# Optimization experiments

Measured on AMD Instinct MI355X. Metric: run time of the kernel, lower is better.

Reference implementation:

```python
import jax, jax.numpy as jnp
import numpy as np

L = 3            # max degree for L_in = L_edge = L_out = (0, 3)
B = 1024         # batch (number of edges)
C_IN = 256
C_OUT = 256
NUM_ORDERS = (L + 1) ** 2  # 16


def _build_structure(L):
    """Rebuild the coo_CG sparse structure: nonzeros sorted by (M_out, l1, l2),
    using the CG selection rule m1 + m2 = m for valid triangle triples."""
    triples = {}
    for l1 in range(L + 1):
        for l2 in range(L + 1):
            for l in range(abs(l1 - l2), min(L, l1 + l2) + 1):
                key = (l, l1, l2)
                if key not in triples:
                    triples[key] = len(triples)
    M1, M2, seg1, lind_g, seg2 = [], [], [], [], []
    g = 0
    for l in range(L + 1):
        for m in range(-l, l + 1):
            M = l * l + l + m  # flat order index of (l, m)
            for (lo, l1, l2) in sorted(triples.keys()):
                if lo != l:
                    continue
                cnt = 0
                for m1 in range(-l1, l1 + 1):
                    m2 = m - m1
                    if -l2 <= m2 <= l2:
                        M1.append(l1 * l1 + l1 + m1)
                        M2.append(l2 * l2 + l2 + m2)
                        seg1.append(g)
                        cnt += 1
                if cnt > 0:
                    lind_g.append(triples[(lo, l1, l2)])
                    seg2.append(M)
                    g += 1
    return (np.asarray(M1, np.int32), np.asarray(M2, np.int32),
            np.asarray(seg1, np.int32), np.asarray(lind_g, np.int32),
            np.asarray(seg2, np.int32), len(triples), g)


def setup_inputs() -> dict:
    key = jax.random.key(0)
    k1, k2, k3, k4 = jax.random.split(key, 4)
    M1, M2, seg1, l_ind, seg2, n_w, n_g = _build_structure(L)
    # expected: 478 nnz, 156 groups, 34 weights
    x = jax.random.normal(k1, (B, NUM_ORDERS, C_IN), jnp.float32)
    sh = jax.random.normal(k2, (B, NUM_ORDERS), jnp.float32)
    fan = np.sqrt(2.0 / (C_IN + C_OUT)).astype(np.float32)
    weight = jax.random.normal(k3, (n_w, C_IN, C_OUT), jnp.float32) * fan
    CG_vals = jax.random.normal(k4, (M1.shape[0],), jnp.float32) * 0.3
    return {
        'x': x, 'sh': sh, 'weight': weight, 'CG_vals': CG_vals,
        'M1': jnp.asarray(M1), 'M2': jnp.asarray(M2), 'seg1': jnp.asarray(seg1),
        'l_ind': jnp.asarray(l_ind), 'seg2': jnp.asarray(seg2),
        'num_orders_out': NUM_ORDERS,
    }


def reference(x, sh, weight, CG_vals, M1, M2, seg1, l_ind, seg2, num_orders_out):
    # x: (B, Mi, Ci); sh: (B, Me); weight: (num_weights, Ci, Co)
    Bn = x.shape[0]
    G = l_ind.shape[0]
    Ci = x.shape[-1]
    Co = weight.shape[-1]
    feat = x[:, M1, :]                                      # (B, nnz, Ci) gather on orders
    sh_g = sh[:, M2]                                        # (B, nnz)
    inter = (CG_vals[None, :] * sh_g)[..., None] * feat     # (B, nnz, Ci)
    inter = jnp.zeros((Bn, G, Ci), x.dtype).at[:, seg1, :].add(inter)   # segment over (M,l1,l2)
    w = weight[l_ind]                                       # (G, Ci, Co)
    ret = jnp.einsum('bgi,gio->bgo', inter, w)              # per-group matmul
    out = jnp.zeros((Bn, num_orders_out, Co), x.dtype).at[:, seg2, :].add(ret)  # segment over M
    return out
```

## Files before the change

### kernel.cpp

```cpp
#include <hip/hip_runtime.h>
#include <stdint.h>

#define B_SZ 1024
#define NO   16
#define CI   256
#define CO   256
#define BK   64
#define BM   32
#define LDB  72
#define LDAA 264
#define MAXG 12
#define MAXE 48
#define WP   76

typedef unsigned short u16;
typedef __attribute__((ext_vector_type(8))) short short8;
typedef __attribute__((ext_vector_type(4))) float f32x4;
typedef __attribute__((ext_vector_type(4))) unsigned short u16x4;
typedef __attribute__((ext_vector_type(8))) unsigned short u16x8;

__device__ __forceinline__ u16 f2bf(float f) {
  union { float f; uint32_t u; } v; v.f = f;
  uint32_t u = v.u;
  return (u16)((u + 0x7FFFu + ((u >> 16) & 1u)) >> 16);
}
__device__ __forceinline__ float bf2f(u16 h) {
  union { float f; uint32_t u; } v; v.u = ((uint32_t)h) << 16; return v.f;
}

__device__ __forceinline__ f32x4 mfma_16x16x32_bf16(short8 a, short8 b, f32x4 c) {
  asm volatile("v_mfma_f32_16x16x32_bf16 %0, %1, %2, %0" : "+v"(c) : "v"(a), "v"(b));
  return c;
}

extern "C" __global__ void xconv_kernel(const float* __restrict__ x,
                                        u16* __restrict__ xbf, int n8) {
  int t = blockIdx.x * 256 + threadIdx.x;
  if (t >= n8) return;
  const float* s = x + (size_t)t * 8;
  float4 a = ((const float4*)s)[0];
  float4 b = ((const float4*)s)[1];
  u16x8 pk;
  pk[0] = f2bf(a.x); pk[1] = f2bf(a.y); pk[2] = f2bf(a.z); pk[3] = f2bf(a.w);
  pk[4] = f2bf(b.x); pk[5] = f2bf(b.y); pk[6] = f2bf(b.z); pk[7] = f2bf(b.w);
  *(u16x8*)(xbf + (size_t)t * 8) = pk;
}

extern "C" __global__ void wconv_kernel(const float* __restrict__ w,
                                        u16* __restrict__ wbf) {
  __shared__ u16 t_lds[64 * WP];
  const int tid = threadIdx.x;
  const int bid = blockIdx.x;
  const int wi = bid >> 4;
  const int i0 = ((bid >> 2) & 3) * 64;
  const int o0 = (bid & 3) * 64;
  const float* src = w + (size_t)wi * (CI * CO);
  u16* dst = wbf + (size_t)wi * (CI * CO);
#pragma unroll
  for (int p = 0; p < 4; ++p) {
    int idx = p * 256 + tid;
    int i = idx >> 4, oq = (idx & 15) * 4;
    float4 v = *(const float4*)(src + (size_t)(i0 + i) * CO + o0 + oq);
    t_lds[(oq + 0) * WP + i] = f2bf(v.x);
    t_lds[(oq + 1) * WP + i] = f2bf(v.y);
    t_lds[(oq + 2) * WP + i] = f2bf(v.z);
    t_lds[(oq + 3) * WP + i] = f2bf(v.w);
  }
  __syncthreads();
#pragma unroll
  for (int p = 0; p < 4; ++p) {
    int idx = p * 256 + tid;
    int o = idx >> 4, iq = (idx & 15) * 4;
    u16x4 v;
    v[0] = t_lds[o * WP + iq + 0]; v[1] = t_lds[o * WP + iq + 1];
    v[2] = t_lds[o * WP + iq + 2]; v[3] = t_lds[o * WP + iq + 3];
    *(u16x4*)(dst + (size_t)(o0 + o) * CI + i0 + iq) = v;
  }
}

extern "C" __global__ void __launch_bounds__(256)
__attribute__((amdgpu_waves_per_eu(4, 4)))
so3_main(const u16* __restrict__ xbf,
         const float* __restrict__ sh,
         const float* __restrict__ CG,
         const u16* __restrict__ wbf,
         const int* __restrict__ M1,
         const int* __restrict__ M2,
         const int* __restrict__ seg1,
         const int* __restrict__ lind,
         const int* __restrict__ seg2,
         float* __restrict__ out,
         int G, int nnz) {
  __shared__ u16 As[BM * LDAA];
  __shared__ u16 Bs[128 * LDB];
  __shared__ u16 coefs[MAXE][BM];
  __shared__ int s_meta[4];
  __shared__ int s_estart[MAXG], s_eend[MAXG], s_wind[MAXG], s_m1[MAXE];

  const int tid = threadIdx.x;
  const int bid = blockIdx.x;
  const int b0  = (bid & 31) * BM;
  const int M   = (bid >> 5) & 15;
  const int co0 = (bid >> 9) * 128;

  if (tid == 0) { s_meta[0] = 1 << 30; s_meta[1] = 0; s_meta[2] = 1 << 30; s_meta[3] = 0; }
  if (tid < MAXG) { s_estart[tid] = 1 << 30; s_eend[tid] = 0; }
  if (tid < MAXE) s_m1[tid] = 0;
  __syncthreads();
  for (int g = tid; g < G; g += 256)
    if (seg2[g] == M) { atomicMin(&s_meta[0], g); atomicMax(&s_meta[1], g + 1); }
  __syncthreads();
  const int gstart = s_meta[0];
  const int ng = s_meta[1] - gstart;
  for (int e = tid; e < nnz; e += 256) {
    int g = seg1[e] - gstart;
    if (g >= 0 && g < ng) {
      atomicMin(&s_meta[2], e); atomicMax(&s_meta[3], e + 1);
      atomicMin(&s_estart[g], e); atomicMax(&s_eend[g], e + 1);
    }
  }
  __syncthreads();
  const int e0 = s_meta[2];
  const int ne = s_meta[3] - e0;
  for (int i = tid; i < ng; i += 256) s_wind[i] = lind[gstart + i];
  for (int i = tid; i < ne; i += 256) s_m1[i] = M1[e0 + i];
  for (int idx = tid; idx < ne * BM; idx += 256) {
    int el = idx / BM, r = idx & (BM - 1);
    int e = e0 + el;
    coefs[el][r] = f2bf(CG[e] * sh[(size_t)(b0 + r) * NO + M2[e]]);
  }
  __syncthreads();

  const int lane = tid & 63;
  const int wn = tid >> 6;
  const int lrow = lane & 15, lq = lane >> 4;
  const int ar = tid >> 3;
  const int ak = (tid & 7) * 8;
  u16* bsw = &Bs[wn * 32 * LDB];

  f32x4 acc[2][2];
#pragma unroll
  for (int i = 0; i < 2; ++i)
#pragma unroll
    for (int j = 0; j < 2; ++j) acc[i][j] = (f32x4){0.f, 0.f, 0.f, 0.f};

  auto buildA = [&](int gl) {
    const int ea = s_estart[gl] - e0;
    const int cnt = (s_eend[gl] - e0) - ea;
    const u16* xb = xbf + (size_t)(b0 + ar) * (NO * CI) + ak;
    float cf[8]; int mo[8];
    const int mo0 = s_m1[ea] * CI;
#pragma unroll
    for (int j = 0; j < 8; ++j) {
      bool v = j < cnt;
      cf[j] = v ? bf2f(coefs[ea + j][ar]) : 0.f;
      mo[j] = v ? s_m1[ea + j] * CI : mo0;
    }
#pragma unroll
    for (int h = 0; h < 2; ++h) {
      float ax[2][8];
#pragma unroll
      for (int q = 0; q < 2; ++q)
#pragma unroll
        for (int j = 0; j < 8; ++j) ax[q][j] = 0.f;
#pragma unroll
      for (int p = 0; p < 4; ++p) {
        if (2 * p < cnt) {
          u16x8 vX[2], vY[2];
#pragma unroll
          for (int q = 0; q < 2; ++q) vX[q] = *(const u16x8*)(xb + mo[2 * p] + (2 * h + q) * 64);
#pragma unroll
          for (int q = 0; q < 2; ++q) vY[q] = *(const u16x8*)(xb + mo[2 * p + 1] + (2 * h + q) * 64);
          const float c0 = cf[2 * p], c1 = cf[2 * p + 1];
#pragma unroll
          for (int q = 0; q < 2; ++q)
#pragma unroll
            for (int j = 0; j < 8; ++j)
              ax[q][j] = fmaf(c1, bf2f((u16)vY[q][j]),
                         fmaf(c0, bf2f((u16)vX[q][j]), ax[q][j]));
        }
      }
#pragma unroll
      for (int q = 0; q < 2; ++q) {
        u16x8 pk;
#pragma unroll
        for (int j = 0; j < 8; ++j) pk[j] = f2bf(ax[q][j]);
        *(u16x8*)&As[ar * LDAA + (2 * h + q) * 64 + ak] = pk;
      }
    }
  };

  u16x8 breg[4];
  auto loadB = [&](int gl, int kkB) {
    const u16* wbn = wbf + (size_t)s_wind[gl] * (CI * CO)
                   + (size_t)(co0 + wn * 32) * CI + kkB;
#pragma unroll
    for (int rr = 0; rr < 4; ++rr) {
      int idx = lane + rr * 64, o = idx >> 3, ic = (idx & 7) * 8;
      breg[rr] = *(const u16x8*)(wbn + (size_t)o * CI + ic);
    }
  };

  loadB(0, 0);
  const int T = ng * 4;

  for (int gl = 0; gl < ng; ++gl) {
    __syncthreads();
    buildA(gl);
    __syncthreads();
#pragma unroll
    for (int kk = 0; kk < 4; ++kk) {
#pragma unroll
      for (int rr = 0; rr < 4; ++rr) {
        int idx = lane + rr * 64, o = idx >> 3, ic = (idx & 7) * 8;
        *(u16x8*)&bsw[o * LDB + ic] = breg[rr];
      }
      {
        int tn = gl * 4 + kk + 1; if (tn >= T) tn = T - 1;
        loadB(tn >> 2, (tn & 3) * BK);
      }
#pragma unroll
      for (int ks = 0; ks < 2; ++ks) {
        short8 af[2], bfr[2];
#pragma unroll
        for (int mf = 0; mf < 2; ++mf)
          af[mf] = *(const short8*)&As[(mf * 16 + lrow) * LDAA + kk * 64 + ks * 32 + lq * 8];
#pragma unroll
        for (int nf = 0; nf < 2; ++nf)
          bfr[nf] = *(const short8*)&bsw[(nf * 16 + lrow) * LDB + ks * 32 + lq * 8];
#pragma unroll
        for (int mf = 0; mf < 2; ++mf)
#pragma unroll
          for (int nf = 0; nf < 2; ++nf)
            acc[mf][nf] = mfma_16x16x32_bf16(af[mf], bfr[nf], acc[mf][nf]);
      }
    }
  }

#pragma unroll
  for (int mf = 0; mf < 2; ++mf) {
    int brow = b0 + mf * 16 + lq * 4;
#pragma unroll
    for (int nf = 0; nf < 2; ++nf) {
      int o = co0 + wn * 32 + nf * 16 + lrow;
#pragma unroll
      for (int rg = 0; rg < 4; ++rg)
        out[(size_t)(brow + rg) * (NO * CO) + (size_t)M * CO + o] = acc[mf][nf][rg];
    }
  }
}

extern "C" void kernel_launch(void* const* d_in, const int* in_sizes, int n_in,
                              void* d_out, int out_size, void* d_ws, size_t ws_size,
                              hipStream_t stream) {
  const float* x   = (const float*)d_in[0];
  const float* sh  = (const float*)d_in[1];
  const float* wgt = (const float*)d_in[2];
  const float* CG  = (const float*)d_in[3];
  const int* M1    = (const int*)d_in[4];
  const int* M2    = (const int*)d_in[5];
  const int* seg1  = (const int*)d_in[6];
  const int* lind  = (const int*)d_in[7];
  const int* seg2  = (const int*)d_in[8];
  float* out       = (float*)d_out;

  const int nnz = in_sizes[3];
  const int G   = in_sizes[7];
  const int n_w = in_sizes[2] / (CI * CO);

  u16* xbf = (u16*)d_ws;
  u16* wbf = (u16*)((char*)d_ws + (size_t)B_SZ * NO * CI * 2);

  int n8 = B_SZ * NO * CI / 8;
  xconv_kernel<<<dim3(n8 / 256), dim3(256), 0, stream>>>(x, xbf, n8);
  wconv_kernel<<<dim3(n_w * 16), dim3(256), 0, stream>>>(wgt, wbf);
  so3_main<<<dim3(1024), dim3(256), 0, stream>>>(xbf, sh, CG, wbf, M1, M2, seg1, lind, seg2,
                                                 out, G, nnz);
}
```

Baseline: 159.0 us.

## Load weights directly into MFMA registers and double-buffer A tile

```diff
diff --git a/kernel.cpp b/kernel.cpp
--- a/kernel.cpp
+++ b/kernel.cpp
@@ -7,7 +7,6 @@
 #define CO   256
 #define BK   64
 #define BM   32
-#define LDB  72
 #define LDAA 264
 #define MAXG 12
 #define MAXE 48
@@ -91,8 +90,7 @@
          const int* __restrict__ seg2,
          float* __restrict__ out,
          int G, int nnz) {
-  __shared__ u16 As[BM * LDAA];
-  __shared__ u16 Bs[128 * LDB];
+  __shared__ u16 As[2 * BM * LDAA];
   __shared__ u16 coefs[MAXE][BM];
   __shared__ int s_meta[4];
   __shared__ int s_estart[MAXG], s_eend[MAXG], s_wind[MAXG], s_m1[MAXE];
@@ -136,7 +134,6 @@
   const int lrow = lane & 15, lq = lane >> 4;
   const int ar = tid >> 3;
   const int ak = (tid & 7) * 8;
-  u16* bsw = &Bs[wn * 32 * LDB];
 
   f32x4 acc[2][2];
 #pragma unroll
@@ -144,7 +141,10 @@
 #pragma unroll
     for (int j = 0; j < 2; ++j) acc[i][j] = (f32x4){0.f, 0.f, 0.f, 0.f};
 
+  const int T = ng * 4;
+
   auto buildA = [&](int gl) {
+    u16* Ad = As + (gl & 1) * (BM * LDAA);
     const int ea = s_estart[gl] - e0;
     const int cnt = (s_eend[gl] - e0) - ea;
     const u16* xb = xbf + (size_t)(b0 + ar) * (NO * CI) + ak;
@@ -185,56 +185,52 @@
         u16x8 pk;
 #pragma unroll
         for (int j = 0; j < 8; ++j) pk[j] = f2bf(ax[q][j]);
-        *(u16x8*)&As[ar * LDAA + (2 * h + q) * 64 + ak] = pk;
+        *(u16x8*)&Ad[ar * LDAA + (2 * h + q) * 64 + ak] = pk;
       }
     }
   };
 
-  u16x8 breg[4];
-  auto loadB = [&](int gl, int kkB) {
-    const u16* wbn = wbf + (size_t)s_wind[gl] * (CI * CO)
-                   + (size_t)(co0 + wn * 32) * CI + kkB;
-#pragma unroll
-    for (int rr = 0; rr < 4; ++rr) {
-      int idx = lane + rr * 64, o = idx >> 3, ic = (idx & 7) * 8;
-      breg[rr] = *(const u16x8*)(wbn + (size_t)o * CI + ic);
-    }
+  auto loadBf = [&](int t, short8* dst) {
+    if (t >= T) t = T - 1;
+    int g = t >> 2, kkB = (t & 3) * BK;
+    const u16* wb = wbf + (size_t)s_wind[g] * (CI * CO)
+                  + (size_t)(co0 + wn * 32) * CI + kkB;
+#pragma unroll
+    for (int nf = 0; nf < 2; ++nf)
+#pragma unroll
+      for (int ks = 0; ks < 2; ++ks)
+        dst[nf * 2 + ks] =
+            *(const short8*)(wb + (size_t)(nf * 16 + lrow) * CI + ks * 32 + lq * 8);
   };
 
-  loadB(0, 0);
-  const int T = ng * 4;
+  auto mma = [&](const u16* Ab, int kk, const short8* bc) {
+#pragma unroll
+    for (int ks = 0; ks < 2; ++ks) {
+      short8 af[2];
+#pragma unroll
+      for (int mf = 0; mf < 2; ++mf)
+        af[mf] = *(const short8*)&Ab[(mf * 16 + lrow) * LDAA + kk * 64 + ks * 32 + lq * 8];
+#pragma unroll
+      for (int mf = 0; mf < 2; ++mf)
+#pragma unroll
+        for (int nf = 0; nf < 2; ++nf)
+          acc[mf][nf] = mfma_16x16x32_bf16(af[mf], bc[nf * 2 + ks], acc[mf][nf]);
+    }
+  };
+
+  short8 bA[4], bB[4];
+  loadBf(0, bA);
+  buildA(0);
 
   for (int gl = 0; gl < ng; ++gl) {
     __syncthreads();
-    buildA(gl);
-    __syncthreads();
-#pragma unroll
-    for (int kk = 0; kk < 4; ++kk) {
-#pragma unroll
-      for (int rr = 0; rr < 4; ++rr) {
-        int idx = lane + rr * 64, o = idx >> 3, ic = (idx & 7) * 8;
-        *(u16x8*)&bsw[o * LDB + ic] = breg[rr];
-      }
-      {
-        int tn = gl * 4 + kk + 1; if (tn >= T) tn = T - 1;
-        loadB(tn >> 2, (tn & 3) * BK);
-      }
-#pragma unroll
-      for (int ks = 0; ks < 2; ++ks) {
-        short8 af[2], bfr[2];
-#pragma unroll
-        for (int mf = 0; mf < 2; ++mf)
-          af[mf] = *(const short8*)&As[(mf * 16 + lrow) * LDAA + kk * 64 + ks * 32 + lq * 8];
-#pragma unroll
-        for (int nf = 0; nf < 2; ++nf)
-          bfr[nf] = *(const short8*)&bsw[(nf * 16 + lrow) * LDB + ks * 32 + lq * 8];
-#pragma unroll
-        for (int mf = 0; mf < 2; ++mf)
-#pragma unroll
-          for (int nf = 0; nf < 2; ++nf)
-            acc[mf][nf] = mfma_16x16x32_bf16(af[mf], bfr[nf], acc[mf][nf]);
-      }
-    }
+    if (gl + 1 < ng) buildA(gl + 1);
+    const u16* Ab = As + (gl & 1) * (BM * LDAA);
+    const int t0 = gl * 4;
+    loadBf(t0 + 1, bB);  mma(Ab, 0, bA);
+    loadBf(t0 + 2, bA);  mma(Ab, 1, bB);
+    loadBf(t0 + 3, bB);  mma(Ab, 2, bA);
+    loadBf(t0 + 4, bA);  mma(Ab, 3, bB);
   }
 
 #pragma unroll
```

After: 200.0 us. +25.8%, slower.
